# Performance work log

Hardware: AMD Instinct MI355X
Metric: run time of the kernel (lower is better)

The kernel has to match this reference:

```python
import jax, jax.numpy as jnp
import numpy as np

NL, NS, NE = 16, 256, 100   # nlatent, nspatial, n_embd
B, P, T = 2, 2, 12


def _xavier(key, shape):
    # torch xavier_uniform: fan_in = shape[1]*prod(rest), fan_out = shape[0]*prod(rest)
    rf = int(np.prod(shape[2:])) if len(shape) > 2 else 1
    fan_in, fan_out = shape[1] * rf, shape[0] * rf
    b = float(np.sqrt(6.0 / (fan_in + fan_out)))
    return jax.random.uniform(key, shape, jnp.float32, -b, b)


def setup_inputs() -> dict:
    key = jax.random.key(0)
    ks = jax.random.split(key, 8)
    x = jax.random.normal(ks[0], (B, P, T, NL, NS), jnp.float32)
    K = _xavier(ks[1], (NS, NS, NL))
    Q = _xavier(ks[2], (NS, NS, NL))
    V = _xavier(ks[3], (NS, NS, NL))
    Aoo = jnp.ones((NS, NS), jnp.float32)
    # Ann is initialized to zeros in the module; use nonzero values so the
    # clamped geometric recurrence over time is actually exercised.
    Ann = jax.random.uniform(ks[4], (NE,), jnp.float32, -0.9, 0.9)
    Aon = _xavier(ks[5], (NS, NS, NE))
    Ano = _xavier(ks[6], (NS, NS, NE))
    w = jnp.ones((NS,), jnp.float32) / NS
    return {"x": x, "K": K, "Q": Q, "V": V, "Aoo": Aoo,
            "Ann": Ann, "Aon": Aon, "Ano": Ano, "w": w}


def reference(x, K, Q, V, Aoo, Ann, Aon, Ano, w):
    # kvt[B,p,T,X,Y] = sum_{x,c} Q[Y,x,c] K[X,x,c] x[B,p,T,c,x]
    kvt = jnp.einsum('Yxc,Xxc,BpTcx->BpTXY', Q, K, x)
    Aon_c = jnp.clip(Aon, -1.0, 1.0)
    Ano_c = jnp.clip(Ano, -1.0, 1.0)

    # t = T-1 term (elementwise Aoo) and t = T-2 term
    h = Aoo[None, None, None] * kvt[:, :, -1:]
    h = h + jnp.einsum('xyn,XYn,BpTXY->BpTxy', Aon_c, Ano_c, kvt[:, :, -2:-1])

    nT = x.shape[2]
    # Ann sequence used in the loop: A_2 = Ann (raw), A_{j+1} = clip(A_j * Ann)
    def step(a, _):
        return jnp.clip(a * Ann, -1.0, 1.0), a
    _, A_seq = jax.lax.scan(step, Ann, None, length=nT - 2)  # [T-2, n], A_seq[j-2]=A_j

    # loop index j=2..T-1 touches time slice t = T-1-j, i.e. t = T-3 .. 0
    s = jnp.einsum('XYn,BpJXY->BpJn', Ano_c, kvt[:, :, :nT - 2])  # J = t in 0..T-3
    A_t = A_seq[::-1]                       # align A_j with time index t = T-1-j
    s2 = jnp.einsum('Jn,BpJn->Bpn', A_t, s)
    h = h + jnp.einsum('xyn,Bpn->Bpxy', Aon_c, s2)[:, :, None]  # [B,p,1,x,y]

    q = jnp.einsum('Xxc,Bpcx->BpcX', V, x[:, :, -1])
    y = jnp.einsum('x,BpcX,BpTXx->BpTc', w, q, h)  # [B,p,1,c]
    return y
```

## Files before the change

kernel.cpp:

```cpp
#include <hip/hip_runtime.h>
#include <hip/hip_fp16.h>


using f32x4 = __attribute__((ext_vector_type(4))) float;
using half8 = __attribute__((ext_vector_type(8))) _Float16;
using half4 = __attribute__((ext_vector_type(4))) _Float16;

#define KVT_STRIDE 3145728ull
#define KS 4

__device__ inline float clip1(float v) { return fminf(fmaxf(v, -1.f), 1.f); }

__device__ inline half8 mul8(uint4 a, uint4 b) {
    half8 x = __builtin_bit_cast(half8, a);
    half8 y = __builtin_bit_cast(half8, b);
    return x * y;
}

__device__ __forceinline__ void gl_lds16(const void* g, void* l) {
    __builtin_amdgcn_global_load_lds(
        (const __attribute__((address_space(1))) void*)g,
        (__attribute__((address_space(3))) void*)l, 16, 0, 0);
}

__global__ void prep_kernel(const float* __restrict__ K, const float* __restrict__ Q,
                            const float* __restrict__ xin,
                            __half* __restrict__ Kh, __half* __restrict__ Qh,
                            __half* __restrict__ u_t)
{
    int b = blockIdx.x, t = threadIdx.x;
    if (b < 512) {
        bool isK = (b < 256);
        int bb = isK ? b : b - 256;
        size_t base = (size_t)bb * 4096 + t * 16;
        const f32x4* src = (const f32x4*)((isK ? K : Q) + base);
        __half* dst = (isK ? Kh : Qh) + base;
        #pragma unroll
        for (int j = 0; j < 2; ++j) {
            f32x4 v0 = src[j * 2], v1 = src[j * 2 + 1];
            half8 h;
            h[0] = (_Float16)v0.x; h[1] = (_Float16)v0.y;
            h[2] = (_Float16)v0.z; h[3] = (_Float16)v0.w;
            h[4] = (_Float16)v1.x; h[5] = (_Float16)v1.y;
            h[6] = (_Float16)v1.z; h[7] = (_Float16)v1.w;
            *(half8*)(dst + j * 8) = h;
        }
    } else {
        int bt = b - 512;
        const float* src = xin + (size_t)bt * 4096;
        int xx = t;
        half8 lo, hi;
        #pragma unroll
        for (int c = 0; c < 8; ++c)  lo[c] = (_Float16)src[c * 256 + xx];
        #pragma unroll
        for (int c = 0; c < 8; ++c)  hi[c] = (_Float16)src[(c + 8) * 256 + xx];
        half8* dst = (half8*)(u_t + (size_t)bt * 4096 + xx * 16);
        dst[0] = lo; dst[1] = hi;
    }
}

__global__ __launch_bounds__(256, 4) void gemm_kvt(
    const __half* __restrict__ Kh, const __half* __restrict__ Qh,
    const __half* __restrict__ u_t, __half* __restrict__ kvtp)
{
    __shared__ __half As[2][128][32];
    __shared__ __half Bs[2][128][32];
    __shared__ __half u_s[1024];

    int bid = blockIdx.x;
    int work = (bid & 7) * 96 + (bid >> 3);
    int kc = work / 192;
    int rem = work - kc * 192;
    int tile = rem / 48;
    int bt = rem - tile * 48;
    int Xb = (tile >> 1) * 128, Yb = (tile & 1) * 128;
    int kbase = kc * 1024;

    int tid = threadIdx.x;
    if (tid < 128)
        *(uint4*)&u_s[tid * 8] = *(const uint4*)(u_t + (size_t)bt * 4096 + kbase + tid * 8);
    __syncthreads();

    int wave = tid >> 6, lane = tid & 63;

    int arow = tid >> 1;
    int apair = (tid & 1) * 2;
    const __half* gA = Kh + (size_t)(Xb + arow) * 4096 + kbase + apair * 8;
    int aswz = (arow >> 1) & 3;
    int asb0 = ((apair + 0) ^ aswz) << 4;
    int asb1 = ((apair + 1) ^ aswz) << 4;

    int srow = lane >> 2;
    int sk = ((lane & 3) ^ ((srow >> 1) & 3)) << 3;
    const __half* gB = Qh + (size_t)(Yb + wave * 16 + srow) * 4096 + kbase + sk;

    int wr = (wave >> 1) * 64, wc = (wave & 1) * 64;
    int lrow = lane & 15, kg = lane >> 4;
    int fb = (kg * 16) ^ (((lrow >> 1) & 3) << 4);

    f32x4 acc[4][4];
    f32x4 zero = {0.f, 0.f, 0.f, 0.f};
    #pragma unroll
    for (int m = 0; m < 4; ++m)
        #pragma unroll
        for (int n = 0; n < 4; ++n) acc[m][n] = zero;

    #define ISSUE_B(s, buf)                                                    \
        do {                                                                   \
            _Pragma("unroll")                                                  \
            for (int i_ = 0; i_ < 2; ++i_)                                     \
                gl_lds16(gB + (size_t)(i_ * 64) * 4096 + (s) * 32,             \
                         &Bs[buf][i_ * 64 + wave * 16][0]);                    \
        } while (0)

    #define WRITE_A(s, r0, r1, buf)                                            \
        do {                                                                   \
            uint4 uv0 = *(const uint4*)&u_s[(s) * 32 + apair * 8];             \
            uint4 uv1 = *(const uint4*)&u_s[(s) * 32 + apair * 8 + 8];         \
            *(half8*)((char*)&As[buf][arow][0] + asb0) = mul8(r0, uv0);        \
            *(half8*)((char*)&As[buf][arow][0] + asb1) = mul8(r1, uv1);        \
        } while (0)

    #define COMPUTE(cur)                                                       \
        do {                                                                   \
            half8 af[4], bf[4];                                                \
            _Pragma("unroll")                                                  \
            for (int m = 0; m < 4; ++m)                                        \
                af[m] = *(const half8*)((const char*)&As[cur][wr + m * 16 + lrow][0] + fb); \
            _Pragma("unroll")                                                  \
            for (int n = 0; n < 4; ++n)                                        \
                bf[n] = *(const half8*)((const char*)&Bs[cur][wc + n * 16 + lrow][0] + fb); \
            _Pragma("unroll")                                                  \
            for (int m = 0; m < 4; ++m)                                        \
                _Pragma("unroll")                                              \
                for (int n = 0; n < 4; ++n)                                    \
                    acc[m][n] = __builtin_amdgcn_mfma_f32_16x16x32_f16(af[m], bf[n], acc[m][n], 0, 0, 0); \
        } while (0)

    #define STEP(s, c0, c1, i0, i1, cur)                                       \
        do {                                                                   \
            if ((s) < 31) asm volatile("s_waitcnt vmcnt(4) lgkmcnt(0)" ::: "memory"); \
            else          asm volatile("s_waitcnt vmcnt(0) lgkmcnt(0)" ::: "memory"); \
            __builtin_amdgcn_s_barrier();                                      \
            __builtin_amdgcn_sched_barrier(0);                                 \
            COMPUTE(cur);                                                      \
            asm volatile("s_waitcnt lgkmcnt(0)" ::: "memory");                 \
            __builtin_amdgcn_s_barrier();                                      \
            __builtin_amdgcn_sched_barrier(0);                                 \
            if ((s) + 2 < 32) {                                                \
                const __half* a_ = gA + ((s) + 2) * 32;                        \
                i0 = *(const uint4*)a_;                                        \
                i1 = *(const uint4*)(a_ + 8);                                  \
                ISSUE_B((s) + 2, cur);                                         \
            }                                                                  \
            if ((s) + 1 < 32) WRITE_A((s) + 1, c0, c1, (cur) ^ 1);             \
        } while (0)

    uint4 aP0, aP1, aC0, aC1;
    aP0 = *(const uint4*)gA;
    aP1 = *(const uint4*)(gA + 8);
    ISSUE_B(0, 0);
    aC0 = *(const uint4*)(gA + 32);
    aC1 = *(const uint4*)(gA + 40);
    ISSUE_B(1, 1);
    WRITE_A(0, aP0, aP1, 0);

    #pragma unroll
    for (int s = 0; s < 32; s += 2) {
        STEP(s,     aC0, aC1, aP0, aP1, 0);
        STEP(s + 1, aP0, aP1, aC0, aC1, 1);
    }
    #undef STEP
    #undef COMPUTE
    #undef WRITE_A
    #undef ISSUE_B

    __half* outp = kvtp + (size_t)kc * KVT_STRIDE + (size_t)bt * 65536;
    int row0 = Xb + wr + kg * 4;
    int col0 = Yb + wc + lrow;
    #pragma unroll
    for (int m = 0; m < 4; ++m)
        #pragma unroll
        for (int n = 0; n < 4; ++n)
            #pragma unroll
            for (int rr = 0; rr < 4; ++rr)
                outp[(size_t)(row0 + m * 16 + rr) * 256 + col0 + n * 16] =
                    __float2half(acc[m][n][rr]);
}

__global__ __launch_bounds__(256) void mid_kernel(
    const float* __restrict__ Ano, const __half* __restrict__ kvtp,
    const float* __restrict__ V, const float* __restrict__ xin,
    const float* __restrict__ Aon, const float* __restrict__ wv,
    float* __restrict__ Sp, float* __restrict__ R, float* __restrict__ W2p)
{
    __shared__ __align__(16) char smem[24896];
    int b = blockIdx.x, tid = threadIdx.x;

    if (b < 1024) {
        __half* anoH = (__half*)smem;
        float (*kvt_s)[68] = (float(*)[68])(smem + 12928);
        int cb = b;
        int k0 = cb * 64;

        {
            const f32x4* src = (const f32x4*)(Ano + (size_t)k0 * 100);
            for (int i = tid; i < 1600; i += 256) {
                f32x4 f = __builtin_nontemporal_load(src + i);
                half4 h;
                h[0] = (_Float16)clip1(f.x); h[1] = (_Float16)clip1(f.y);
                h[2] = (_Float16)clip1(f.z); h[3] = (_Float16)clip1(f.w);
                *(half4*)&anoH[i * 4] = h;
            }
        }
        {
            for (int idx = tid; idx < 352; idx += 256) {
                int rI = idx >> 3, g = idx & 7;
                int bpr = rI / 11, Jr = rI - bpr * 11;
                const __half* p = kvtp + (size_t)(bpr * 12 + Jr) * 65536 + k0 + g * 8;
                half8 v0 = *(const half8*)(p);
                half8 v1 = *(const half8*)(p + KVT_STRIDE);
                half8 v2 = *(const half8*)(p + 2 * KVT_STRIDE);
                half8 v3 = *(const half8*)(p + 3 * KVT_STRIDE);
                f32x4 lo, hi;
                #pragma unroll
                for (int j = 0; j < 4; ++j) {
                    lo[j] = (float)v0[j] + (float)v1[j] + (float)v2[j] + (float)v3[j];
                    hi[j] = (float)v0[j+4] + (float)v1[j+4] + (float)v2[j+4] + (float)v3[j+4];
                }
                *(f32x4*)&kvt_s[rI][g * 8]     = lo;
                *(f32x4*)&kvt_s[rI][g * 8 + 4] = hi;
            }
        }
        __syncthreads();

        int lane = tid & 63;
        int bp = tid >> 6;
        bool has2 = lane < 36;
        float acc0[11], acc1[11];
        #pragma unroll
        for (int J = 0; J < 11; ++J) { acc0[J] = 0.f; acc1[J] = 0.f; }

        for (int k = 0; k < 64; k += 4) {
            f32x4 kv[11];
            #pragma unroll
            for (int J = 0; J < 11; ++J)
                kv[J] = *(const f32x4*)&kvt_s[bp * 11 + J][k];
            #pragma unroll
            for (int kk = 0; kk < 4; ++kk) {
                float a0 = (float)anoH[(k + kk) * 100 + lane];
                float a1r = (float)anoH[(k + kk) * 100 + 64 + lane];
                float a1 = has2 ? a1r : 0.f;
                #pragma unroll
                for (int J = 0; J < 11; ++J) {
                    acc0[J] += kv[J][kk] * a0;
                    acc1[J] += kv[J][kk] * a1;
                }
            }
        }
        float* outb = Sp + ((size_t)cb * 4 + bp) * 1100;
        #pragma unroll
        for (int J = 0; J < 11; ++J) {
            outb[J * 100 + lane] = acc0[J];
            if (has2) outb[J * 100 + 64 + lane] = acc1[J];
        }
    } else if (b < 1280) {
        float* vrow = (float*)smem;
        int X = b - 1024;
        {
            const float4* src = (const float4*)(V + (size_t)X * 4096);
            float4* dst = (float4*)vrow;
            for (int i = tid; i < 1024; i += 256) dst[i] = src[i];
        }
        __syncthreads();
        int bp = tid >> 6, c = (tid >> 2) & 15, g = tid & 3;
        const float* xl = xin + ((size_t)(bp * 12) + 11) * 4096 + c * 256;
        float p = 0.f;
        #pragma unroll 4
        for (int x = g * 64; x < g * 64 + 64; ++x)
            p += xl[x] * vrow[x * 16 + c];
        p += __shfl_xor(p, 1);
        p += __shfl_xor(p, 2);
        if (g == 0) R[((size_t)bp * 256 + X) * 16 + c] = p;
    } else {
        int idx = b - 1280;
        int X = idx >> 1, h = idx & 1;
        int g = h * 2 + (tid >> 7), n = tid & 127;
        if (n < 100) {
            const float* base = Aon + (size_t)X * 25600 + (size_t)g * 6400 + n;
            float acc = 0.f;
            for (int bb = 0; bb < 64; ++bb)
                acc += wv[g * 64 + bb] * clip1(__builtin_nontemporal_load(base + (size_t)bb * 100));
            W2p[((size_t)g * 256 + X) * 100 + n] = acc;
        }
    }
}

__global__ void reduce_s(const float* __restrict__ Sp, float* __restrict__ Sq,
                         float* __restrict__ out)
{
    int bid = blockIdx.x;
    int t = threadIdx.x;
    if (bid == 0 && t < 64) out[t] = 0.f;
    int qq = bid & 7, idx = bid >> 3;
    int bp = idx / 11, J = idx - bp * 11;
    if (t >= 100) return;
    float acc = 0.f;
    for (int c = qq * 128; c < qq * 128 + 128; ++c)
        acc += Sp[((size_t)c * 4 + bp) * 1100 + J * 100 + t];
    Sq[(size_t)(qq * 44 + idx) * 100 + t] = acc;
}

__global__ __launch_bounds__(256) void hw_kernel(const float* __restrict__ Aoo,
                                                 const float* __restrict__ wv,
                                                 const __half* __restrict__ kvtp,
                                                 const float* __restrict__ W2p,
                                                 const float* __restrict__ Sq,
                                                 const float* __restrict__ Ann,
                                                 const float* __restrict__ R,
                                                 float* __restrict__ out)
{
    __shared__ float yp[4][16];
    __shared__ float c2s[128];
    int bp = blockIdx.x >> 6, Xg = blockIdx.x & 63;
    int tid = threadIdx.x;

    if (tid < 128) {
        int n = tid;
        float r = 0.f;
        if (n < 100) {
            float S[11];
            #pragma unroll
            for (int J = 0; J < 11; ++J) {
                float s = 0.f;
                #pragma unroll
                for (int qq = 0; qq < 8; ++qq)
                    s += Sq[(size_t)(qq * 44 + bp * 11 + J) * 100 + n];
                S[J] = s;
            }
            float a = Ann[n];
            float seq[10];
            float v = a;
            seq[0] = v;
            #pragma unroll
            for (int s2 = 1; s2 < 10; ++s2) { v = clip1(v * a); seq[s2] = v; }
            r = S[10];
            #pragma unroll
            for (int J = 0; J < 10; ++J)
                r += seq[9 - J] * S[J];
        }
        c2s[n] = r;
    }
    __syncthreads();

    int wave = tid >> 6, lane = tid & 63;
    int X = Xg * 4 + wave;
    size_t base = (size_t)(bp * 12 + 11) * 65536 + (size_t)X * 256;
    const float* ao = Aoo + (size_t)X * 256;
    float red = 0.f;
    #pragma unroll
    for (int qq = 0; qq < 4; ++qq) {
        int xx = qq * 64 + lane;
        float kvv = 0.f;
        #pragma unroll
        for (int c = 0; c < KS; ++c)
            kvv += __half2float(kvtp[(size_t)c * KVT_STRIDE + base + xx]);
        red += wv[xx] * ao[xx] * kvv;
    }
    float w2a = 0.f, w2b = 0.f;
    #pragma unroll
    for (int g = 0; g < 4; ++g) {
        w2a += W2p[((size_t)g * 256 + X) * 100 + lane];
        if (lane < 36) w2b += W2p[((size_t)g * 256 + X) * 100 + 64 + lane];
    }
    red += c2s[lane] * w2a;
    if (lane < 36)
        red += c2s[64 + lane] * w2b;
    #pragma unroll
    for (int off = 32; off; off >>= 1) red += __shfl_xor(red, off);
    if (lane < 16) yp[wave][lane] = red * R[((size_t)bp * 256 + X) * 16 + lane];
    __syncthreads();
    if (tid < 16) {
        float s = yp[0][tid] + yp[1][tid] + yp[2][tid] + yp[3][tid];
        atomicAdd(&out[bp * 16 + tid], s);
    }
}

extern "C" void kernel_launch(void* const* d_in, const int* in_sizes, int n_in,
                              void* d_out, int out_size, void* d_ws, size_t ws_size,
                              hipStream_t stream)
{
    const float* x   = (const float*)d_in[0];
    const float* K   = (const float*)d_in[1];
    const float* Q   = (const float*)d_in[2];
    const float* V   = (const float*)d_in[3];
    const float* Aoo = (const float*)d_in[4];
    const float* Ann = (const float*)d_in[5];
    const float* Aon = (const float*)d_in[6];
    const float* Ano = (const float*)d_in[7];
    const float* wv  = (const float*)d_in[8];
    float* out = (float*)d_out;

    char* ws = (char*)d_ws;
    const size_t o_Qh   = 0;
    const size_t o_Kh   = o_Qh + (size_t)2 * 1024 * 1024;
    const size_t o_ut   = o_Kh + (size_t)2 * 1024 * 1024;
    const size_t o_kvtp = o_ut + (size_t)512 * 1024;
    const size_t o_Sp   = o_kvtp + (size_t)KS * KVT_STRIDE * 2;
    const size_t o_Sq   = o_Sp + (size_t)1024 * 4400 * 4;
    const size_t o_W2   = o_Sq + (size_t)35200 * 4 + 64;
    const size_t o_R    = o_W2 + (size_t)102400 * 4;

    __half* Qh  = (__half*)(ws + o_Qh);
    __half* Kh  = (__half*)(ws + o_Kh);
    __half* u_t = (__half*)(ws + o_ut);
    __half* kvtp = (__half*)(ws + o_kvtp);
    float* Sp   = (float*)(ws + o_Sp);
    float* Sq   = (float*)(ws + o_Sq);
    float* W2p  = (float*)(ws + o_W2);
    float* R    = (float*)(ws + o_R);

    hipLaunchKernelGGL(prep_kernel, dim3(560),  dim3(256), 0, stream,
                       K, Q, x, Kh, Qh, u_t);
    hipLaunchKernelGGL(gemm_kvt,    dim3(768),  dim3(256), 0, stream,
                       Kh, Qh, u_t, kvtp);
    hipLaunchKernelGGL(mid_kernel,  dim3(1792), dim3(256), 0, stream,
                       Ano, kvtp, V, x, Aon, wv, Sp, R, W2p);
    hipLaunchKernelGGL(reduce_s,    dim3(352),  dim3(128), 0, stream, Sp, Sq, out);
    hipLaunchKernelGGL(hw_kernel,   dim3(256),  dim3(256), 0, stream,
                       Aoo, wv, kvtp, W2p, Sq, Ann, R, out);
}
```

Before: 94.03 us.

## Double-buffer Ano/kvt chunks in mid_kernel and cut partial-sum count fourfold

After: 88.95 us. 5.4% less time.

```diff
diff --git a/kernel.cpp b/kernel.cpp
--- a/kernel.cpp
+++ b/kernel.cpp
@@ -194,45 +194,15 @@
     const float* __restrict__ Aon, const float* __restrict__ wv,
     float* __restrict__ Sp, float* __restrict__ R, float* __restrict__ W2p)
 {
-    __shared__ __align__(16) char smem[24896];
+    __shared__ __align__(16) char smem[49792];
     int b = blockIdx.x, tid = threadIdx.x;
 
-    if (b < 1024) {
-        __half* anoH = (__half*)smem;
-        float (*kvt_s)[68] = (float(*)[68])(smem + 12928);
-        int cb = b;
-        int k0 = cb * 64;
-
-        {
-            const f32x4* src = (const f32x4*)(Ano + (size_t)k0 * 100);
-            for (int i = tid; i < 1600; i += 256) {
-                f32x4 f = __builtin_nontemporal_load(src + i);
-                half4 h;
-                h[0] = (_Float16)clip1(f.x); h[1] = (_Float16)clip1(f.y);
-                h[2] = (_Float16)clip1(f.z); h[3] = (_Float16)clip1(f.w);
-                *(half4*)&anoH[i * 4] = h;
-            }
-        }
-        {
-            for (int idx = tid; idx < 352; idx += 256) {
-                int rI = idx >> 3, g = idx & 7;
-                int bpr = rI / 11, Jr = rI - bpr * 11;
-                const __half* p = kvtp + (size_t)(bpr * 12 + Jr) * 65536 + k0 + g * 8;
-                half8 v0 = *(const half8*)(p);
-                half8 v1 = *(const half8*)(p + KVT_STRIDE);
-                half8 v2 = *(const half8*)(p + 2 * KVT_STRIDE);
-                half8 v3 = *(const half8*)(p + 3 * KVT_STRIDE);
-                f32x4 lo, hi;
-                #pragma unroll
-                for (int j = 0; j < 4; ++j) {
-                    lo[j] = (float)v0[j] + (float)v1[j] + (float)v2[j] + (float)v3[j];
-                    hi[j] = (float)v0[j+4] + (float)v1[j+4] + (float)v2[j+4] + (float)v3[j+4];
-                }
-                *(f32x4*)&kvt_s[rI][g * 8]     = lo;
-                *(f32x4*)&kvt_s[rI][g * 8 + 4] = hi;
-            }
-        }
-        __syncthreads();
+    if (b < 256) {
+        __half* anoA = (__half*)smem;
+        __half* anoB = (__half*)(smem + 12928);
+        float (*kvtA)[68] = (float(*)[68])(smem + 25856);
+        float (*kvtB)[68] = (float(*)[68])(smem + 37824);
+        int k0 = b * 256;
 
         int lane = tid & 63;
         int bp = tid >> 6;
@@ -241,32 +211,117 @@
         #pragma unroll
         for (int J = 0; J < 11; ++J) { acc0[J] = 0.f; acc1[J] = 0.f; }
 
-        for (int k = 0; k < 64; k += 4) {
-            f32x4 kv[11];
-            #pragma unroll
-            for (int J = 0; J < 11; ++J)
-                kv[J] = *(const f32x4*)&kvt_s[bp * 11 + J][k];
-            #pragma unroll
-            for (int kk = 0; kk < 4; ++kk) {
-                float a0 = (float)anoH[(k + kk) * 100 + lane];
-                float a1r = (float)anoH[(k + kk) * 100 + 64 + lane];
-                float a1 = has2 ? a1r : 0.f;
-                #pragma unroll
-                for (int J = 0; J < 11; ++J) {
-                    acc0[J] += kv[J][kk] * a0;
-                    acc1[J] += kv[J][kk] * a1;
-                }
-            }
-        }
-        float* outb = Sp + ((size_t)cb * 4 + bp) * 1100;
+        f32x4 ar[7];
+        half8 kr[2][4];
+
+        #define LOAD_SP(cc)                                                    \
+            do {                                                               \
+                int k0s = k0 + (cc) * 64;                                      \
+                const f32x4* asrc = (const f32x4*)(Ano + (size_t)k0s * 100);   \
+                _Pragma("unroll")                                              \
+                for (int it = 0; it < 7; ++it) {                               \
+                    int i = tid + it * 256;                                    \
+                    if (i < 1600) ar[it] = __builtin_nontemporal_load(asrc + i); \
+                }                                                              \
+                _Pragma("unroll")                                              \
+                for (int it = 0; it < 2; ++it) {                               \
+                    int idx = tid + it * 256;                                  \
+                    if (idx < 352) {                                           \
+                        int rI = idx >> 3, g = idx & 7;                        \
+                        int bpr = rI / 11, Jr = rI - bpr * 11;                 \
+                        const __half* p = kvtp + (size_t)(bpr * 12 + Jr) * 65536 + k0s + g * 8; \
+                        kr[it][0] = *(const half8*)(p);                        \
+                        kr[it][1] = *(const half8*)(p + KVT_STRIDE);           \
+                        kr[it][2] = *(const half8*)(p + 2 * KVT_STRIDE);       \
+                        kr[it][3] = *(const half8*)(p + 3 * KVT_STRIDE);       \
+                    }                                                          \
+                }                                                              \
+            } while (0)
+
+        #define WRITE_SP(anoDst, kvtDst)                                       \
+            do {                                                               \
+                _Pragma("unroll")                                              \
+                for (int it = 0; it < 7; ++it) {                               \
+                    int i = tid + it * 256;                                    \
+                    if (i < 1600) {                                            \
+                        half4 h;                                               \
+                        h[0] = (_Float16)clip1(ar[it].x);                      \
+                        h[1] = (_Float16)clip1(ar[it].y);                      \
+                        h[2] = (_Float16)clip1(ar[it].z);                      \
+                        h[3] = (_Float16)clip1(ar[it].w);                      \
+                        *(half4*)&anoDst[i * 4] = h;                           \
+                    }                                                          \
+                }                                                              \
+                _Pragma("unroll")                                              \
+                for (int it = 0; it < 2; ++it) {                               \
+                    int idx = tid + it * 256;                                  \
+                    if (idx < 352) {                                           \
+                        int rI = idx >> 3, g = idx & 7;                        \
+                        f32x4 lo, hi;                                          \
+                        _Pragma("unroll")                                      \
+                        for (int j = 0; j < 4; ++j) {                          \
+                            lo[j] = (float)kr[it][0][j] + (float)kr[it][1][j]  \
+                                  + (float)kr[it][2][j] + (float)kr[it][3][j]; \
+                            hi[j] = (float)kr[it][0][j+4] + (float)kr[it][1][j+4] \
+                                  + (float)kr[it][2][j+4] + (float)kr[it][3][j+4]; \
+                        }                                                      \
+                        *(f32x4*)&kvtDst[rI][g * 8]     = lo;                  \
+                        *(f32x4*)&kvtDst[rI][g * 8 + 4] = hi;                  \
+                    }                                                          \
+                }                                                              \
+            } while (0)
+
+        #define COMPUTE_SP(anoSrc, kvtSrc)                                     \
+            do {                                                               \
+                for (int k = 0; k < 64; k += 4) {                              \
+                    f32x4 kv[11];                                              \
+                    _Pragma("unroll")                                          \
+                    for (int J = 0; J < 11; ++J)                               \
+                        kv[J] = *(const f32x4*)&kvtSrc[bp * 11 + J][k];        \
+                    _Pragma("unroll")                                          \
+                    for (int kk = 0; kk < 4; ++kk) {                           \
+                        float a0 = (float)anoSrc[(k + kk) * 100 + lane];       \
+                        float a1r = (float)anoSrc[(k + kk) * 100 + 64 + lane]; \
+                        float a1 = has2 ? a1r : 0.f;                           \
+                        _Pragma("unroll")                                      \
+                        for (int J = 0; J < 11; ++J) {                         \
+                            acc0[J] += kv[J][kk] * a0;                         \
+                            acc1[J] += kv[J][kk] * a1;                         \
+                        }                                                      \
+                    }                                                          \
+                }                                                              \
+            } while (0)
+
+        LOAD_SP(0);
+        WRITE_SP(anoA, kvtA);
+        __syncthreads();
+        LOAD_SP(1);
+        COMPUTE_SP(anoA, kvtA);
+        WRITE_SP(anoB, kvtB);
+        __syncthreads();
+        LOAD_SP(2);
+        COMPUTE_SP(anoB, kvtB);
+        WRITE_SP(anoA, kvtA);
+        __syncthreads();
+        LOAD_SP(3);
+        COMPUTE_SP(anoA, kvtA);
+        WRITE_SP(anoB, kvtB);
+        __syncthreads();
+        COMPUTE_SP(anoB, kvtB);
+
+        #undef LOAD_SP
+        #undef WRITE_SP
+        #undef COMPUTE_SP
+
+        float* outb = Sp + ((size_t)b * 4 + bp) * 1100;
         #pragma unroll
         for (int J = 0; J < 11; ++J) {
             outb[J * 100 + lane] = acc0[J];
             if (has2) outb[J * 100 + 64 + lane] = acc1[J];
         }
-    } else if (b < 1280) {
+    } else if (b < 512) {
         float* vrow = (float*)smem;
-        int X = b - 1024;
+        int X = b - 256;
         {
             const float4* src = (const float4*)(V + (size_t)X * 4096);
             float4* dst = (float4*)vrow;
@@ -283,7 +338,7 @@
         p += __shfl_xor(p, 2);
         if (g == 0) R[((size_t)bp * 256 + X) * 16 + c] = p;
     } else {
-        int idx = b - 1280;
+        int idx = b - 512;
         int X = idx >> 1, h = idx & 1;
         int g = h * 2 + (tid >> 7), n = tid & 127;
         if (n < 100) {
@@ -306,7 +361,7 @@
     int bp = idx / 11, J = idx - bp * 11;
     if (t >= 100) return;
     float acc = 0.f;
-    for (int c = qq * 128; c < qq * 128 + 128; ++c)
+    for (int c = qq * 32; c < qq * 32 + 32; ++c)
         acc += Sp[((size_t)c * 4 + bp) * 1100 + J * 100 + t];
     Sq[(size_t)(qq * 44 + idx) * 100 + t] = acc;
 }
@@ -407,7 +462,7 @@
     const size_t o_ut   = o_Kh + (size_t)2 * 1024 * 1024;
     const size_t o_kvtp = o_ut + (size_t)512 * 1024;
     const size_t o_Sp   = o_kvtp + (size_t)KS * KVT_STRIDE * 2;
-    const size_t o_Sq   = o_Sp + (size_t)1024 * 4400 * 4;
+    const size_t o_Sq   = o_Sp + (size_t)256 * 4400 * 4;
     const size_t o_W2   = o_Sq + (size_t)35200 * 4 + 64;
     const size_t o_R    = o_W2 + (size_t)102400 * 4;
 
@@ -424,7 +479,7 @@
                        K, Q, x, Kh, Qh, u_t);
     hipLaunchKernelGGL(gemm_kvt,    dim3(768),  dim3(256), 0, stream,
                        Kh, Qh, u_t, kvtp);
-    hipLaunchKernelGGL(mid_kernel,  dim3(1792), dim3(256), 0, stream,
+    hipLaunchKernelGGL(mid_kernel,  dim3(1024), dim3(256), 0, stream,
                        Ano, kvtp, V, x, Aon, wv, Sp, R, W2p);
     hipLaunchKernelGGL(reduce_s,    dim3(352),  dim3(128), 0, stream, Sp, Sq, out);
     hipLaunchKernelGGL(hw_kernel,   dim3(256),  dim3(256), 0, stream,
```
